# Performance work log

Measured on AMD Instinct MI355X. Metric: run time of the kernel, lower is better.

The kernel has to match this reference:

```python
import jax, jax.numpy as jnp
import numpy as np

N_NODES = 50000
N_EDGES = 600000
ATOM_DIM = 75
HID = 128
N_LAYERS = 4
OUT_DIM = 1
NUM_GRAPHS = 128
EPS = 1e-5


def _bn(x, gamma, beta):
    # BatchNorm1d training-mode forward (biased variance)
    mu = jnp.mean(x, axis=0)
    var = jnp.mean((x - mu) ** 2, axis=0)
    return (x - mu) * jax.lax.rsqrt(var + EPS) * gamma + beta


def setup_inputs() -> dict:
    key = jax.random.key(0)
    ks = jax.random.split(key, 24)
    s = 0.05
    inp = {
        'node_features': jax.random.normal(ks[0], (N_NODES, ATOM_DIM), jnp.float32),
        'edge_index': jax.random.randint(ks[1], (2, N_EDGES), 0, N_NODES, jnp.int32),
        'batch_idx': jnp.sort(jax.random.randint(ks[2], (N_NODES,), 0, NUM_GRAPHS, jnp.int32)),
        # atom embedding: Linear(75->128) + ReLU + BN
        'emb_W': jax.random.normal(ks[3], (HID, ATOM_DIM), jnp.float32) * s,
        'emb_b': jnp.zeros((HID,), jnp.float32),
        'emb_g': jnp.ones((HID,), jnp.float32),
        'emb_beta': jnp.zeros((HID,), jnp.float32),
        # per-layer params, stacked over L=4
        'msg_W': jax.random.normal(ks[4], (N_LAYERS, HID, HID), jnp.float32) * s,
        'msg_b': jnp.zeros((N_LAYERS, HID), jnp.float32),
        'att_W': jax.random.normal(ks[5], (N_LAYERS, 2 * HID), jnp.float32) * s,
        'att_b': jnp.zeros((N_LAYERS,), jnp.float32),
        'gru_Wih': jax.random.normal(ks[6], (N_LAYERS, 3 * HID, HID), jnp.float32) * s,
        'gru_bih': jnp.zeros((N_LAYERS, 3 * HID), jnp.float32),
        'gru_Whh': jax.random.normal(ks[7], (N_LAYERS, 3 * HID, HID), jnp.float32) * s,
        'gru_bhh': jnp.zeros((N_LAYERS, 3 * HID), jnp.float32),
        'bn_g': jnp.ones((N_LAYERS, HID), jnp.float32),
        'bn_b': jnp.zeros((N_LAYERS, HID), jnp.float32),
        # readout: Linear(128->64) + ReLU + Linear(64->1)
        'ro_W1': jax.random.normal(ks[8], (HID // 2, HID), jnp.float32) * s,
        'ro_b1': jnp.zeros((HID // 2,), jnp.float32),
        'ro_W2': jax.random.normal(ks[9], (OUT_DIM, HID // 2), jnp.float32) * s,
        'ro_b2': jnp.zeros((OUT_DIM,), jnp.float32),
    }
    return inp


def _forward(node_features, edge_index, batch_idx, emb_W, emb_b, emb_g, emb_beta,
             msg_W, msg_b, att_W, att_b, gru_Wih, gru_bih, gru_Whh, gru_bhh,
             bn_g, bn_b, ro_W1, ro_b1, ro_W2, ro_b2):
    src, dst = edge_index[0], edge_index[1]
    # atom embedding
    x = _bn(jax.nn.relu(node_features @ emb_W.T + emb_b), emb_g, emb_beta)
    for l in range(N_LAYERS):
        xs = x[src]                                   # [E, h] gather
        xd = x[dst]                                   # [E, h] gather
        ef = jnp.concatenate([xs, xd], axis=1)        # [E, 2h]
        att = jax.nn.sigmoid(ef @ att_W[l] + att_b[l])  # [E]
        msgs = (xs @ msg_W[l].T + msg_b[l]) * att[:, None]  # [E, h]
        agg = jax.ops.segment_sum(msgs, dst, num_segments=N_NODES)  # [N, h]
        # GRUCell(agg, x)
        gi = agg @ gru_Wih[l].T + gru_bih[l]
        gh = x @ gru_Whh[l].T + gru_bhh[l]
        i_r, i_z, i_n = jnp.split(gi, 3, axis=1)
        h_r, h_z, h_n = jnp.split(gh, 3, axis=1)
        r = jax.nn.sigmoid(i_r + h_r)
        z = jax.nn.sigmoid(i_z + h_z)
        n = jnp.tanh(i_n + r * h_n)
        h_new = (1.0 - z) * n + z * x
        x = _bn(h_new, bn_g[l], bn_b[l])              # dropout is identity in eval
    # graph readout: sum-pool per graph
    graph_repr = jax.ops.segment_sum(x, batch_idx, num_segments=NUM_GRAPHS)  # [G, h]
    h1 = jax.nn.relu(graph_repr @ ro_W1.T + ro_b1)
    return h1 @ ro_W2.T + ro_b2                       # [G, 1]


def reference(node_features, edge_index, batch_idx, emb_W, emb_b, emb_g, emb_beta,
              msg_W, msg_b, att_W, att_b, gru_Wih, gru_bih, gru_Whh, gru_bhh,
              bn_g, bn_b, ro_W1, ro_b1, ro_W2, ro_b2):
    return _forward(node_features, edge_index, batch_idx, emb_W, emb_b, emb_g, emb_beta,
                    msg_W, msg_b, att_W, att_b, gru_Wih, gru_bih, gru_Whh, gru_bhh,
                    bn_g, bn_b, ro_W1, ro_b1, ro_W2, ro_b2)
```

## Files before the change

### kernel.cpp

```cpp
#include <hip/hip_runtime.h>
#include <math.h>

#define NN 50000
#define NE 600000
#define ADIM 75
#define HID 128
#define NLAYERS 4
#define NGRAPHS 128
#define BN_EPS 1e-5f
#define NNP 50048
#define NB64 (NNP / 64)

typedef short bhalf8 __attribute__((ext_vector_type(8)));
typedef float floatx4 __attribute__((ext_vector_type(4)));

__device__ __forceinline__ float sigm(float v) { return 1.0f / (1.0f + __expf(-v)); }
__device__ __forceinline__ float tanh_f(float v) {
    return 1.0f - 2.0f / (__expf(2.0f * v) + 1.0f);
}

__device__ __forceinline__ unsigned short f2bf(float f) {
    unsigned u = __builtin_bit_cast(unsigned, f);
    u = (u + 0x7FFFu + ((u >> 16) & 1u)) >> 16;
    return (unsigned short)u;
}
__device__ __forceinline__ float bf2f(unsigned short h) {
    return __builtin_bit_cast(float, ((unsigned)h) << 16);
}

__device__ __forceinline__ void gl2lds16(const void* g, void* l) {
    __builtin_amdgcn_global_load_lds(
        (const __attribute__((address_space(1))) unsigned int*)g,
        (__attribute__((address_space(3))) unsigned int*)l, 16, 0, 0);
}

__global__ __launch_bounds__(256) void k_nfb(
    const float* __restrict__ nf, unsigned short* __restrict__ nfb)
{
    int e = blockIdx.x * 256 + threadIdx.x;
    if (e >= NN * 24) return;
    int n = e / 24, k4 = e - n * 24;
    ushort4 o;
    int k = k4 * 4;
    o.x = (k + 0 < ADIM) ? f2bf(nf[(size_t)n * ADIM + k + 0]) : 0;
    o.y = (k + 1 < ADIM) ? f2bf(nf[(size_t)n * ADIM + k + 1]) : 0;
    o.z = (k + 2 < ADIM) ? f2bf(nf[(size_t)n * ADIM + k + 2]) : 0;
    o.w = (k + 3 < ADIM) ? f2bf(nf[(size_t)n * ADIM + k + 3]) : 0;
    ((ushort4*)nfb)[(size_t)n * 24 + k4] = o;
}

__global__ __launch_bounds__(256) void k_wfrag_emb(
    const float* __restrict__ W, unsigned short* __restrict__ web)
{
    int e = blockIdx.x * 256 + threadIdx.x;
    int j = e & 7, n = (e >> 3) & 15, quad = (e >> 7) & 3;
    int kb = (e >> 9) % 3, tc = e / 1536;
    int row = tc * 16 + n;
    int kk = kb * 32 + quad * 8 + j;
    web[e] = (kk < ADIM) ? f2bf(W[row * ADIM + kk]) : 0;
}

__global__ __launch_bounds__(256) void k_embed_m(
    const unsigned short* __restrict__ nfb, const unsigned short* __restrict__ web,
    const float* __restrict__ b, float* __restrict__ y,
    double* __restrict__ bnsum)
{
    __shared__ __align__(16) unsigned short wbe[12288];
    __shared__ float sred[512], sred2[512];
    const int t = threadIdx.x;
    const int wave = t >> 6, lane = t & 63;
    const int col = lane & 15, quad = (lane >> 4) & 3;
    const int node0 = blockIdx.x * 64;

    {
        const char* gsrc = (const char*)web + wave * 6144 + lane * 16;
        char* ldst = (char*)wbe + wave * 6144;
#pragma unroll
        for (int i = 0; i < 6; i++)
            gl2lds16(gsrc + i * 1024, ldst + i * 1024);
    }

    const int anode = node0 + wave * 16 + col;
    bhalf8 afN[3];
#pragma unroll
    for (int kb = 0; kb < 3; kb++)
        afN[kb] = *(const bhalf8*)&nfb[(size_t)anode * 96 + kb * 32 + quad * 8];

    floatx4 acc[8];
#pragma unroll
    for (int tc = 0; tc < 8; tc++) {
        float bv = b[tc * 16 + col];
        acc[tc] = (floatx4){bv, bv, bv, bv};
    }
    __syncthreads();

#pragma unroll
    for (int tc = 0; tc < 8; tc++) {
        bhalf8 bfr[3];
#pragma unroll
        for (int kb = 0; kb < 3; kb++)
            bfr[kb] = *(const bhalf8*)&wbe[((tc * 3 + kb) * 64 + lane) * 8];
#pragma unroll
        for (int kb = 0; kb < 3; kb++)
            acc[tc] = __builtin_amdgcn_mfma_f32_16x16x32_bf16(afN[kb], bfr[kb], acc[tc], 0, 0, 0);
    }

    float ps[8], ps2[8];
#pragma unroll
    for (int tc = 0; tc < 8; tc++) {
        ps[tc] = 0.f; ps2[tc] = 0.f;
#pragma unroll
        for (int e = 0; e < 4; e++) {
            float v = fmaxf(acc[tc][e], 0.0f);
            int nd = node0 + wave * 16 + quad * 4 + e;
            if (nd < NN) {
                y[(size_t)nd * HID + tc * 16 + col] = v;
                ps[tc] += v; ps2[tc] += v * v;
            }
        }
    }
#pragma unroll
    for (int tc = 0; tc < 8; tc++) {
        ps[tc]  += __shfl_xor(ps[tc], 16);  ps2[tc] += __shfl_xor(ps2[tc], 16);
        ps[tc]  += __shfl_xor(ps[tc], 32);  ps2[tc] += __shfl_xor(ps2[tc], 32);
    }
    if (quad == 0) {
#pragma unroll
        for (int tc = 0; tc < 8; tc++) {
            sred[wave * 128 + tc * 16 + col]  = ps[tc];
            sred2[wave * 128 + tc * 16 + col] = ps2[tc];
        }
    }
    __syncthreads();
    if (t < 128) {
        float s  = sred[t]  + sred[128 + t]  + sred[256 + t]  + sred[384 + t];
        float s2 = sred2[t] + sred2[128 + t] + sred2[256 + t] + sred2[384 + t];
        unsafeAtomicAdd(&bnsum[t], (double)s);
        unsafeAtomicAdd(&bnsum[128 + t], (double)s2);
    }
}

__global__ __launch_bounds__(256) void k_bnx(
    const float* __restrict__ y, const double* __restrict__ bnsum,
    const float* __restrict__ g, const float* __restrict__ beta,
    const float* __restrict__ attW,
    unsigned short* __restrict__ xb,
    float* __restrict__ as_, float* __restrict__ ad_)
{
    const int t = threadIdx.x;
    const int n = blockIdx.x * 4 + (t >> 6);
    const int lane = t & 63;
    const int f0 = lane * 2;
    double m0 = bnsum[f0] / (double)NN;
    double v0 = bnsum[128 + f0] / (double)NN - m0 * m0;
    double m1 = bnsum[f0 + 1] / (double)NN;
    double v1 = bnsum[128 + f0 + 1] / (double)NN - m1 * m1;
    float sc0 = g[f0] * rsqrtf((float)v0 + BN_EPS);
    float sc1 = g[f0 + 1] * rsqrtf((float)v1 + BN_EPS);
    float sh0 = beta[f0] - (float)m0 * sc0;
    float sh1 = beta[f0 + 1] - (float)m1 * sc1;

    float2 v = ((const float2*)y)[(size_t)n * 64 + lane];
    float2 xv;
    xv.x = v.x * sc0 + sh0;
    xv.y = v.y * sc1 + sh1;
    unsigned pk = (unsigned)f2bf(xv.x) | ((unsigned)f2bf(xv.y) << 16);
    ((unsigned*)xb)[(size_t)n * 64 + lane] = pk;
    float2 aws = ((const float2*)attW)[lane];
    float2 awd = ((const float2*)(attW + 128))[lane];
    float pas = xv.x * aws.x + xv.y * aws.y;
    float pad = xv.x * awd.x + xv.y * awd.y;
#pragma unroll
    for (int msk = 32; msk >= 1; msk >>= 1) {
        pas += __shfl_xor(pas, msk);
        pad += __shfl_xor(pad, msk);
    }
    if (lane == 0) { as_[n] = pas; ad_[n] = pad; }
}

__global__ __launch_bounds__(128) void k_wc(
    const float* __restrict__ Wih, const float* __restrict__ Wm,
    const float* __restrict__ bm, float* __restrict__ Wc, float* __restrict__ bmih)
{
    __shared__ float sw[128];
    __shared__ float red[128];
    const int b = blockIdx.x;
    const int l = b / 384, r = b - l * 384;
    const int t = threadIdx.x;
    const float* wihrow = Wih + ((size_t)l * 384 + r) * 128;
    sw[t] = wihrow[t];
    __syncthreads();
    const float* wm = Wm + (size_t)l * 128 * 128;
    float acc = 0.f;
#pragma unroll 8
    for (int k = 0; k < 128; k++) acc += sw[k] * wm[k * 128 + t];
    Wc[((size_t)l * 384 + r) * 128 + t] = acc;
    red[t] = sw[t] * bm[l * 128 + t];
    __syncthreads();
#pragma unroll
    for (int off = 64; off >= 1; off >>= 1) {
        if (t < off) red[t] += red[t + off];
        __syncthreads();
    }
    if (t == 0) bmih[l * 384 + r] = red[0];
}

__global__ __launch_bounds__(256) void k_frag(
    const float* __restrict__ Wc, const float* __restrict__ Whh,
    unsigned short* __restrict__ wcb, unsigned short* __restrict__ whhb)
{
    const int b = blockIdx.x;
    const int mat = b / 192;
    const int e = (b - mat * 192) * 256 + threadIdx.x;
    const int l = mat >> 1, which = mat & 1;
    const float* src = which ? (Whh + (size_t)l * 49152) : (Wc + (size_t)l * 49152);
    unsigned short* dst = which ? (whhb + (size_t)l * 49152) : (wcb + (size_t)l * 49152);
    int j = e & 7, n = (e >> 3) & 15, quad = (e >> 7) & 3;
    int kb = (e >> 9) & 3, tc = (e >> 11) & 7, g = (e >> 14) & 3;
    int row = g * 128 + tc * 16 + n;
    int kk = kb * 32 + quad * 8 + j;
    dst[e] = f2bf(src[row * 128 + kk]);
}

__global__ __launch_bounds__(256) void k_count(const int* __restrict__ dst, int* __restrict__ cnt)
{
    int e = blockIdx.x * 256 + threadIdx.x;
    if (e < NE) atomicAdd(&cnt[dst[e]], 1);
}

#define SCAN_B 512
#define SCAN_G 98

__global__ __launch_bounds__(SCAN_B) void k_scan1(
    const int* __restrict__ cnt, int* __restrict__ rowptr, int* __restrict__ bsum)
{
    __shared__ int s[SCAN_B];
    const int t = threadIdx.x;
    const int i = blockIdx.x * SCAN_B + t;
    int v = (i < NN) ? cnt[i] : 0;
    s[t] = v;
    __syncthreads();
#pragma unroll
    for (int off = 1; off < SCAN_B; off <<= 1) {
        int u = (t >= off) ? s[t - off] : 0;
        __syncthreads();
        s[t] += u;
        __syncthreads();
    }
    if (i < NN) rowptr[i] = s[t] - v;
    if (t == SCAN_B - 1) bsum[blockIdx.x] = s[t];
}

__global__ __launch_bounds__(128) void k_scan2(int* __restrict__ bsum, int* __restrict__ rowptr)
{
    __shared__ int s[128];
    const int t = threadIdx.x;
    int v = (t < SCAN_G) ? bsum[t] : 0;
    s[t] = v;
    __syncthreads();
#pragma unroll
    for (int off = 1; off < 128; off <<= 1) {
        int u = (t >= off) ? s[t - off] : 0;
        __syncthreads();
        s[t] += u;
        __syncthreads();
    }
    if (t < SCAN_G) bsum[t] = s[t] - v;
    if (t == 127) rowptr[NN] = s[127];
}

__global__ __launch_bounds__(SCAN_B) void k_scan3(
    int* __restrict__ rowptr, const int* __restrict__ bsum, int* __restrict__ wptr)
{
    const int i = blockIdx.x * SCAN_B + threadIdx.x;
    if (i < NN) {
        int v = rowptr[i] + bsum[blockIdx.x];
        rowptr[i] = v;
        wptr[i] = v;
    }
}

__global__ __launch_bounds__(256) void k_scatter(
    const int* __restrict__ src, const int* __restrict__ dst,
    int* __restrict__ wptr, int* __restrict__ ssrc)
{
    int e = blockIdx.x * 256 + threadIdx.x;
    if (e < NE) {
        int d = dst[e];
        int pos = atomicAdd(&wptr[d], 1);
        ssrc[pos] = src[e];
    }
}

__global__ __launch_bounds__(256) void k_gather(
    const int* __restrict__ rowptr, const int* __restrict__ ssrc,
    const unsigned short* __restrict__ xb, const float* __restrict__ as_,
    const float* __restrict__ ad_, const float* __restrict__ attb, int l,
    unsigned short* __restrict__ aggxb, float* __restrict__ sumatt)
{
    const int t = threadIdx.x;
    const int n = blockIdx.x * 8 + (t >> 5);
    const int lane = t & 31;
    const int r0 = rowptr[n], r1 = rowptr[n + 1];
    const float adv = ad_[n] + attb[l];
    float4 acc = make_float4(0.f, 0.f, 0.f, 0.f);
    float satt = 0.f;

    int ids[8], ids2[8];
    if (r0 < r1) {
#pragma unroll
        for (int k = 0; k < 8; k++) {
            int idx = r0 + k; if (idx >= r1) idx = r1 - 1;
            ids[k] = ssrc[idx];
        }
    }
    for (int base = r0; base < r1; base += 8) {
        const int nxt = base + 8;
        if (nxt < r1) {
#pragma unroll
            for (int k = 0; k < 8; k++) {
                int idx = nxt + k; if (idx >= r1) idx = r1 - 1;
                ids2[k] = ssrc[idx];
            }
        }
        ushort4 v[8];
        float a[8];
#pragma unroll
        for (int k = 0; k < 8; k++) {
            v[k] = ((const ushort4*)xb)[(size_t)ids[k] * 32 + lane];
            a[k] = as_[ids[k]];
        }
#pragma unroll
        for (int k = 0; k < 8; k++) {
            if (base + k < r1) {
                float att = sigm(a[k] + adv);
                acc.x += bf2f(v[k].x) * att; acc.y += bf2f(v[k].y) * att;
                acc.z += bf2f(v[k].z) * att; acc.w += bf2f(v[k].w) * att;
                satt += att;
            }
        }
#pragma unroll
        for (int k = 0; k < 8; k++) ids[k] = ids2[k];
    }
    ushort4 o;
    o.x = f2bf(acc.x); o.y = f2bf(acc.y); o.z = f2bf(acc.z); o.w = f2bf(acc.w);
    ((ushort4*)aggxb)[(size_t)n * 32 + lane] = o;
    if (lane == 0) sumatt[n] = satt;
}

#define STAGE_W(SRC)                                                          \
    {                                                                         \
        const char* gsrc = (const char*)(SRC) + wave * 8192 + lane * 16;      \
        char* ldst = (char*)wbuf + wave * 8192;                               \
        _Pragma("unroll")                                                     \
        for (int i = 0; i < 8; i++)                                           \
            gl2lds16(gsrc + i * 1024, ldst + i * 1024);                       \
    }

#define MMGL(AF, ACC)                                                         \
    _Pragma("unroll")                                                         \
    for (int tc = 0; tc < 8; tc++) {                                          \
        bhalf8 bfr[4];                                                        \
        _Pragma("unroll")                                                     \
        for (int kb = 0; kb < 4; kb++)                                        \
            bfr[kb] = *(const bhalf8*)&wbuf[((tc * 4 + kb) * 64 + lane) * 8]; \
        _Pragma("unroll")                                                     \
        for (int kb = 0; kb < 4; kb++)                                        \
            ACC[tc] = __builtin_amdgcn_mfma_f32_16x16x32_bf16(AF[kb], bfr[kb], ACC[tc], 0, 0, 0); \
    }

__global__ __launch_bounds__(256) void k_gru(
    const unsigned short* __restrict__ aggxb, const float* __restrict__ sumatt,
    const unsigned short* __restrict__ xb,
    const unsigned short* __restrict__ wcb, const float* __restrict__ bmih,
    const float* __restrict__ bih,
    const unsigned short* __restrict__ whhb, const float* __restrict__ bhh,
    float* __restrict__ y, double* __restrict__ bnsum)
{
    __shared__ __align__(16) unsigned short wbuf[16384];
    __shared__ float sred[512], sred2[512];
    const int t = threadIdx.x;
    const int wave = t >> 6, lane = t & 63;
    const int col = lane & 15, quad = (lane >> 4) & 3;
    const int node0 = blockIdx.x * 64;

    STAGE_W(wcb + 0 * 16384);

    const int anode = node0 + wave * 16 + col;
    bhalf8 afA[4], afX[4];
#pragma unroll
    for (int kb = 0; kb < 4; kb++) {
        afA[kb] = *(const bhalf8*)&aggxb[(size_t)anode * HID + kb * 32 + quad * 8];
        afX[kb] = *(const bhalf8*)&xb[(size_t)anode * HID + kb * 32 + quad * 8];
    }
    float sa[4];
#pragma unroll
    for (int e = 0; e < 4; e++) sa[e] = sumatt[node0 + wave * 16 + quad * 4 + e];

    floatx4 accR[8], accN[8];

#pragma unroll
    for (int tc = 0; tc < 8; tc++) {
        int f = 0 * 128 + tc * 16 + col;
        float b0 = bih[f] + bhh[f], bm = bmih[f];
        accR[tc] = (floatx4){b0 + sa[0] * bm, b0 + sa[1] * bm, b0 + sa[2] * bm, b0 + sa[3] * bm};
    }
    __syncthreads();
    MMGL(afA, accR);
    __syncthreads();
    STAGE_W(whhb + 0 * 16384);
    __syncthreads();
    MMGL(afX, accR);
    __syncthreads();
    STAGE_W(whhb + 2 * 16384);
#pragma unroll
    for (int tc = 0; tc < 8; tc++)
#pragma unroll
        for (int e = 0; e < 4; e++)
            accR[tc][e] = sigm(accR[tc][e]);

#pragma unroll
    for (int tc = 0; tc < 8; tc++) {
        float bh = bhh[2 * 128 + tc * 16 + col];
        accN[tc] = (floatx4){bh, bh, bh, bh};
    }
    __syncthreads();
    MMGL(afX, accN);
    __syncthreads();
    STAGE_W(wcb + 2 * 16384);
#pragma unroll
    for (int tc = 0; tc < 8; tc++) {
        int f = 2 * 128 + tc * 16 + col;
        float bi = bih[f], bm = bmih[f];
#pragma unroll
        for (int e = 0; e < 4; e++)
            accN[tc][e] = accR[tc][e] * accN[tc][e] + bi + sa[e] * bm;
    }
    __syncthreads();
    MMGL(afA, accN);
    __syncthreads();
    STAGE_W(wcb + 1 * 16384);
#pragma unroll
    for (int tc = 0; tc < 8; tc++)
#pragma unroll
        for (int e = 0; e < 4; e++)
            accN[tc][e] = tanh_f(accN[tc][e]);

#pragma unroll
    for (int tc = 0; tc < 8; tc++) {
        int f = 1 * 128 + tc * 16 + col;
        float b0 = bih[f] + bhh[f], bm = bmih[f];
        accR[tc] = (floatx4){b0 + sa[0] * bm, b0 + sa[1] * bm, b0 + sa[2] * bm, b0 + sa[3] * bm};
    }
    __syncthreads();
    MMGL(afA, accR);
    __syncthreads();
    STAGE_W(whhb + 1 * 16384);
    __syncthreads();
    MMGL(afX, accR);

    float ps[8], ps2[8];
#pragma unroll
    for (int tc = 0; tc < 8; tc++) {
        ps[tc] = 0.f; ps2[tc] = 0.f;
#pragma unroll
        for (int e = 0; e < 4; e++) {
            float z = sigm(accR[tc][e]);
            int nd = node0 + wave * 16 + quad * 4 + e;
            float xv = bf2f(xb[(size_t)nd * HID + tc * 16 + col]);
            float h = (1.0f - z) * accN[tc][e] + z * xv;
            if (nd < NN) {
                y[(size_t)nd * HID + tc * 16 + col] = h;
                ps[tc] += h; ps2[tc] += h * h;
            }
        }
    }
#pragma unroll
    for (int tc = 0; tc < 8; tc++) {
        ps[tc]  += __shfl_xor(ps[tc], 16);  ps2[tc] += __shfl_xor(ps2[tc], 16);
        ps[tc]  += __shfl_xor(ps[tc], 32);  ps2[tc] += __shfl_xor(ps2[tc], 32);
    }
    if (quad == 0) {
#pragma unroll
        for (int tc = 0; tc < 8; tc++) {
            sred[wave * 128 + tc * 16 + col]  = ps[tc];
            sred2[wave * 128 + tc * 16 + col] = ps2[tc];
        }
    }
    __syncthreads();
    if (t < 128) {
        float s  = sred[t]  + sred[128 + t]  + sred[256 + t]  + sred[384 + t];
        float s2 = sred2[t] + sred2[128 + t] + sred2[256 + t] + sred2[384 + t];
        unsafeAtomicAdd(&bnsum[t], (double)s);
        unsafeAtomicAdd(&bnsum[128 + t], (double)s2);
    }
}

__global__ __launch_bounds__(256) void k_pool(
    const unsigned short* __restrict__ xb, const int* __restrict__ batch,
    float* __restrict__ gr)
{
    __shared__ int sb[256];
    const int t = threadIdx.x;
    const int nb = blockIdx.x * 256;
    int ld = nb + t; if (ld >= NN) ld = NN - 1;
    sb[t] = batch[ld];
    __syncthreads();
    const int s = t >> 7, f = t & 127;
    float acc = 0.f; int cur = -1;
    for (int i = s; i < 256; i += 2) {
        int n = nb + i;
        if (n >= NN) break;
        int g = sb[i];
        if (g != cur) {
            if (cur >= 0) unsafeAtomicAdd(&gr[(size_t)cur * HID + f], acc);
            acc = 0.f; cur = g;
        }
        acc += bf2f(xb[(size_t)n * HID + f]);
    }
    if (cur >= 0) unsafeAtomicAdd(&gr[(size_t)cur * HID + f], acc);
}

__global__ __launch_bounds__(64) void k_readout(
    const float* __restrict__ gr, const float* __restrict__ W1,
    const float* __restrict__ b1, const float* __restrict__ W2,
    const float* __restrict__ b2, float* __restrict__ out)
{
    const int g = blockIdx.x, j = threadIdx.x;
    float acc = b1[j];
    const float4* grow = (const float4*)&gr[g * HID];
    const float4* wrow = (const float4*)&W1[j * HID];
#pragma unroll
    for (int k4 = 0; k4 < 32; k4++) {
        float4 a = grow[k4], w = wrow[k4];
        acc += a.x * w.x + a.y * w.y + a.z * w.z + a.w * w.w;
    }
    float h = fmaxf(acc, 0.0f) * W2[j];
#pragma unroll
    for (int msk = 32; msk >= 1; msk >>= 1) h += __shfl_xor(h, msk);
    if (j == 0) out[g] = h + b2[0];
}

extern "C" void kernel_launch(void* const* d_in, const int* in_sizes, int n_in,
                              void* d_out, int out_size, void* d_ws, size_t ws_size,
                              hipStream_t stream)
{
    const float* nf    = (const float*)d_in[0];
    const int*   ei    = (const int*)d_in[1];
    const int*   batch = (const int*)d_in[2];
    const float* embW  = (const float*)d_in[3];
    const float* embb  = (const float*)d_in[4];
    const float* embg  = (const float*)d_in[5];
    const float* embbe = (const float*)d_in[6];
    const float* msgW  = (const float*)d_in[7];
    const float* msgb  = (const float*)d_in[8];
    const float* attW  = (const float*)d_in[9];
    const float* attb  = (const float*)d_in[10];
    const float* Wih   = (const float*)d_in[11];
    const float* bih   = (const float*)d_in[12];
    const float* Whh   = (const float*)d_in[13];
    const float* bhh   = (const float*)d_in[14];
    const float* bng   = (const float*)d_in[15];
    const float* bnb   = (const float*)d_in[16];
    const float* roW1  = (const float*)d_in[17];
    const float* rob1  = (const float*)d_in[18];
    const float* roW2  = (const float*)d_in[19];
    const float* rob2  = (const float*)d_in[20];
    const int* src = ei;
    const int* dst = ei + NE;
    float* out = (float*)d_out;

    char* base = (char*)d_ws;
    const size_t NH = (size_t)NN * HID;
    double* bnsum = (double*)base;
    float* y     = (float*)(base + 10240);
    unsigned short* xb    = (unsigned short*)(y + NH);
    unsigned short* aggxb = xb + NH;
    float* as_   = (float*)(aggxb + NH);
    float* ad_   = as_ + NN;
    float* sumatt= ad_ + NN;
    float* gr    = sumatt + NN;
    float* Wc    = gr + NGRAPHS * HID;
    float* bmih  = Wc + 4 * 384 * 128;
    int* rowptr  = (int*)(bmih + 4 * 384);
    int* wptr    = rowptr + NN + 4;
    int* cnt     = wptr + NN;
    int* bsum    = cnt + NN;
    int* ssrc    = bsum + 128;
    unsigned short* wcb  = (unsigned short*)(ssrc + NE);
    unsigned short* whhb = wcb + 4 * 49152;
    unsigned short* nfb  = whhb + 4 * 49152;
    unsigned short* web  = nfb + (size_t)NNP * 96;

    k_wc<<<4 * 384, 128, 0, stream>>>(Wih, msgW, msgb, Wc, bmih);
    k_frag<<<8 * 192, 256, 0, stream>>>(Wc, Whh, wcb, whhb);
    k_nfb<<<(NN * 24 + 255) / 256, 256, 0, stream>>>(nf, nfb);
    k_wfrag_emb<<<48, 256, 0, stream>>>(embW, web);
    hipMemsetAsync(cnt, 0, NN * sizeof(int), stream);
    hipMemsetAsync(bnsum, 0, 5 * 256 * sizeof(double), stream);
    k_count<<<(NE + 255) / 256, 256, 0, stream>>>(dst, cnt);
    k_scan1<<<SCAN_G, SCAN_B, 0, stream>>>(cnt, rowptr, bsum);
    k_scan2<<<1, 128, 0, stream>>>(bsum, rowptr);
    k_scan3<<<SCAN_G, SCAN_B, 0, stream>>>(rowptr, bsum, wptr);
    k_scatter<<<(NE + 255) / 256, 256, 0, stream>>>(src, dst, wptr, ssrc);

    k_embed_m<<<NB64, 256, 0, stream>>>(nfb, web, embb, y, bnsum);
    k_bnx<<<NN / 4, 256, 0, stream>>>(y, bnsum, embg, embbe, attW, xb, as_, ad_);

    for (int l = 0; l < NLAYERS; l++) {
        k_gather<<<NN / 8, 256, 0, stream>>>(rowptr, ssrc, xb, as_, ad_, attb, l, aggxb, sumatt);
        k_gru<<<NB64, 256, 0, stream>>>(
            aggxb, sumatt, xb,
            wcb + (size_t)l * 49152, bmih + (size_t)l * 384, bih + (size_t)l * 384,
            whhb + (size_t)l * 49152, bhh + (size_t)l * 384, y, bnsum + (l + 1) * 256);
        const float* attW_next = attW + (size_t)((l + 1 < NLAYERS) ? l + 1 : l) * 256;
        k_bnx<<<NN / 4, 256, 0, stream>>>(y, bnsum + (l + 1) * 256,
                                          bng + (size_t)l * HID, bnb + (size_t)l * HID,
                                          attW_next, xb, as_, ad_);
    }

    hipMemsetAsync(gr, 0, NGRAPHS * HID * sizeof(float), stream);
    k_pool<<<(NN + 255) / 256, 256, 0, stream>>>(xb, batch, gr);
    k_readout<<<NGRAPHS, 64, 0, stream>>>(gr, roW1, rob1, roW2, rob2, out);
}
```

Measured before the change: 630.3 us.

## Use 128-node blocks for embed/GRU and float BN statistics

Doubles the node tile per block in the embedding and GRU MFMA kernels (512 threads, 8 waves), so each block loads the shared weight fragments once for twice as many nodes. This halves the weight-staging traffic and the number of atomic BN-sum updates. BN sum and sum-of-squares accumulation also moves from double to float atomics and the stats finalize math from double to float. That removes slow FP64 atomics and divides, but E[x^2]-mean^2 in float over 50k nodes can lose precision.

```diff
diff --git a/kernel.cpp b/kernel.cpp
--- a/kernel.cpp
+++ b/kernel.cpp
@@ -9,7 +9,7 @@
 #define NGRAPHS 128
 #define BN_EPS 1e-5f
 #define NNP 50048
-#define NB64 (NNP / 64)
+#define NB128 (NNP / 128)
 
 typedef short bhalf8 __attribute__((ext_vector_type(8)));
 typedef float floatx4 __attribute__((ext_vector_type(4)));
@@ -60,23 +60,23 @@
     web[e] = (kk < ADIM) ? f2bf(W[row * ADIM + kk]) : 0;
 }
 
-__global__ __launch_bounds__(256) void k_embed_m(
+__global__ __launch_bounds__(512) void k_embed_m(
     const unsigned short* __restrict__ nfb, const unsigned short* __restrict__ web,
     const float* __restrict__ b, float* __restrict__ y,
-    double* __restrict__ bnsum)
+    float* __restrict__ bnsum)
 {
     __shared__ __align__(16) unsigned short wbe[12288];
-    __shared__ float sred[512], sred2[512];
+    __shared__ float sred[1024], sred2[1024];
     const int t = threadIdx.x;
     const int wave = t >> 6, lane = t & 63;
     const int col = lane & 15, quad = (lane >> 4) & 3;
-    const int node0 = blockIdx.x * 64;
+    const int node0 = blockIdx.x * 128;
 
     {
-        const char* gsrc = (const char*)web + wave * 6144 + lane * 16;
-        char* ldst = (char*)wbe + wave * 6144;
-#pragma unroll
-        for (int i = 0; i < 6; i++)
+        const char* gsrc = (const char*)web + wave * 3072 + lane * 16;
+        char* ldst = (char*)wbe + wave * 3072;
+#pragma unroll
+        for (int i = 0; i < 3; i++)
             gl2lds16(gsrc + i * 1024, ldst + i * 1024);
     }
 
@@ -133,15 +133,16 @@
     }
     __syncthreads();
     if (t < 128) {
-        float s  = sred[t]  + sred[128 + t]  + sred[256 + t]  + sred[384 + t];
-        float s2 = sred2[t] + sred2[128 + t] + sred2[256 + t] + sred2[384 + t];
-        unsafeAtomicAdd(&bnsum[t], (double)s);
-        unsafeAtomicAdd(&bnsum[128 + t], (double)s2);
+        float s = 0.f, s2 = 0.f;
+#pragma unroll
+        for (int w = 0; w < 8; w++) { s += sred[w * 128 + t]; s2 += sred2[w * 128 + t]; }
+        unsafeAtomicAdd(&bnsum[t], s);
+        unsafeAtomicAdd(&bnsum[128 + t], s2);
     }
 }
 
 __global__ __launch_bounds__(256) void k_bnx(
-    const float* __restrict__ y, const double* __restrict__ bnsum,
+    const float* __restrict__ y, const float* __restrict__ bnsum,
     const float* __restrict__ g, const float* __restrict__ beta,
     const float* __restrict__ attW,
     unsigned short* __restrict__ xb,
@@ -151,14 +152,14 @@
     const int n = blockIdx.x * 4 + (t >> 6);
     const int lane = t & 63;
     const int f0 = lane * 2;
-    double m0 = bnsum[f0] / (double)NN;
-    double v0 = bnsum[128 + f0] / (double)NN - m0 * m0;
-    double m1 = bnsum[f0 + 1] / (double)NN;
-    double v1 = bnsum[128 + f0 + 1] / (double)NN - m1 * m1;
-    float sc0 = g[f0] * rsqrtf((float)v0 + BN_EPS);
-    float sc1 = g[f0 + 1] * rsqrtf((float)v1 + BN_EPS);
-    float sh0 = beta[f0] - (float)m0 * sc0;
-    float sh1 = beta[f0 + 1] - (float)m1 * sc1;
+    float m0 = bnsum[f0] * (1.0f / NN);
+    float v0 = bnsum[128 + f0] * (1.0f / NN) - m0 * m0;
+    float m1 = bnsum[f0 + 1] * (1.0f / NN);
+    float v1 = bnsum[128 + f0 + 1] * (1.0f / NN) - m1 * m1;
+    float sc0 = g[f0] * rsqrtf(v0 + BN_EPS);
+    float sc1 = g[f0 + 1] * rsqrtf(v1 + BN_EPS);
+    float sh0 = beta[f0] - m0 * sc0;
+    float sh1 = beta[f0 + 1] - m1 * sc1;
 
     float2 v = ((const float2*)y)[(size_t)n * 64 + lane];
     float2 xv;
@@ -350,10 +351,10 @@
 
 #define STAGE_W(SRC)                                                          \
     {                                                                         \
-        const char* gsrc = (const char*)(SRC) + wave * 8192 + lane * 16;      \
-        char* ldst = (char*)wbuf + wave * 8192;                               \
+        const char* gsrc = (const char*)(SRC) + wave * 4096 + lane * 16;      \
+        char* ldst = (char*)wbuf + wave * 4096;                               \
         _Pragma("unroll")                                                     \
-        for (int i = 0; i < 8; i++)                                           \
+        for (int i = 0; i < 4; i++)                                           \
             gl2lds16(gsrc + i * 1024, ldst + i * 1024);                       \
     }
 
@@ -369,20 +370,20 @@
             ACC[tc] = __builtin_amdgcn_mfma_f32_16x16x32_bf16(AF[kb], bfr[kb], ACC[tc], 0, 0, 0); \
     }
 
-__global__ __launch_bounds__(256) void k_gru(
+__global__ __launch_bounds__(512) void k_gru(
     const unsigned short* __restrict__ aggxb, const float* __restrict__ sumatt,
     const unsigned short* __restrict__ xb,
     const unsigned short* __restrict__ wcb, const float* __restrict__ bmih,
     const float* __restrict__ bih,
     const unsigned short* __restrict__ whhb, const float* __restrict__ bhh,
-    float* __restrict__ y, double* __restrict__ bnsum)
+    float* __restrict__ y, float* __restrict__ bnsum)
 {
     __shared__ __align__(16) unsigned short wbuf[16384];
-    __shared__ float sred[512], sred2[512];
+    __shared__ float sred[1024], sred2[1024];
     const int t = threadIdx.x;
     const int wave = t >> 6, lane = t & 63;
     const int col = lane & 15, quad = (lane >> 4) & 3;
-    const int node0 = blockIdx.x * 64;
+    const int node0 = blockIdx.x * 128;
 
     STAGE_W(wcb + 0 * 16384);
 
@@ -489,10 +490,11 @@
     }
     __syncthreads();
     if (t < 128) {
-        float s  = sred[t]  + sred[128 + t]  + sred[256 + t]  + sred[384 + t];
-        float s2 = sred2[t] + sred2[128 + t] + sred2[256 + t] + sred2[384 + t];
-        unsafeAtomicAdd(&bnsum[t], (double)s);
-        unsafeAtomicAdd(&bnsum[128 + t], (double)s2);
+        float s = 0.f, s2 = 0.f;
+#pragma unroll
+        for (int w = 0; w < 8; w++) { s += sred[w * 128 + t]; s2 += sred2[w * 128 + t]; }
+        unsafeAtomicAdd(&bnsum[t], s);
+        unsafeAtomicAdd(&bnsum[128 + t], s2);
     }
 }
 
@@ -572,7 +574,7 @@
 
     char* base = (char*)d_ws;
     const size_t NH = (size_t)NN * HID;
-    double* bnsum = (double*)base;
+    float* bnsum = (float*)base;
     float* y     = (float*)(base + 10240);
     unsigned short* xb    = (unsigned short*)(y + NH);
     unsigned short* aggxb = xb + NH;
@@ -597,19 +599,19 @@
     k_nfb<<<(NN * 24 + 255) / 256, 256, 0, stream>>>(nf, nfb);
     k_wfrag_emb<<<48, 256, 0, stream>>>(embW, web);
     hipMemsetAsync(cnt, 0, NN * sizeof(int), stream);
-    hipMemsetAsync(bnsum, 0, 5 * 256 * sizeof(double), stream);
+    hipMemsetAsync(bnsum, 0, 5 * 256 * sizeof(float), stream);
     k_count<<<(NE + 255) / 256, 256, 0, stream>>>(dst, cnt);
     k_scan1<<<SCAN_G, SCAN_B, 0, stream>>>(cnt, rowptr, bsum);
     k_scan2<<<1, 128, 0, stream>>>(bsum, rowptr);
     k_scan3<<<SCAN_G, SCAN_B, 0, stream>>>(rowptr, bsum, wptr);
     k_scatter<<<(NE + 255) / 256, 256, 0, stream>>>(src, dst, wptr, ssrc);
 
-    k_embed_m<<<NB64, 256, 0, stream>>>(nfb, web, embb, y, bnsum);
+    k_embed_m<<<NB128, 512, 0, stream>>>(nfb, web, embb, y, bnsum);
     k_bnx<<<NN / 4, 256, 0, stream>>>(y, bnsum, embg, embbe, attW, xb, as_, ad_);
 
     for (int l = 0; l < NLAYERS; l++) {
         k_gather<<<NN / 8, 256, 0, stream>>>(rowptr, ssrc, xb, as_, ad_, attb, l, aggxb, sumatt);
-        k_gru<<<NB64, 256, 0, stream>>>(
+        k_gru<<<NB128, 512, 0, stream>>>(
             aggxb, sumatt, xb,
             wcb + (size_t)l * 49152, bmih + (size_t)l * 384, bih + (size_t)l * 384,
             whhb + (size_t)l * 49152, bhh + (size_t)l * 384, y, bnsum + (l + 1) * 256);
```

Result: faster. 614.4 us (-2.5%).
